# Performance work log

Hardware: AMD Instinct MI355X
Metric: run time of the kernel (lower is better)

## Reference

```python
import jax, jax.numpy as jnp
import numpy as np

NUM_HEADS = 16


def setup_inputs() -> dict:
    key = jax.random.key(0)
    ks = jax.random.split(key, 5)
    B, S, D = 4, 2048, 1024
    scale = 1.0 / np.sqrt(D)
    return {
        "x": jax.random.normal(ks[0], (B, S, D), dtype=jnp.float32),
        "q_proj": jax.random.normal(ks[1], (D, D), dtype=jnp.float32) * scale,
        "k_proj": jax.random.normal(ks[2], (D, D), dtype=jnp.float32) * scale,
        "v_proj": jax.random.normal(ks[3], (D, D), dtype=jnp.float32) * scale,
        "o_proj": jax.random.normal(ks[4], (D, D), dtype=jnp.float32) * scale,
    }


def reference(x, q_proj, k_proj, v_proj, o_proj):
    B, S, D = x.shape
    H = NUM_HEADS
    hd = D // H
    # projections: weight is [d_out, d_in]
    q = jnp.einsum('bsd,kd->bsk', x, q_proj)
    k = jnp.einsum('bsd,kd->bsk', x, k_proj)
    v = jnp.einsum('bsd,kd->bsk', x, v_proj)
    # split heads: [B, H, S, hd]
    q = q.reshape(B, S, H, hd).transpose(0, 2, 1, 3)
    k = k.reshape(B, S, H, hd).transpose(0, 2, 1, 3)
    v = v.reshape(B, S, H, hd).transpose(0, 2, 1, 3)
    scores = jnp.einsum('bhqd,bhkd->bhqk', q, k) / jnp.sqrt(jnp.asarray(hd, dtype=x.dtype))
    causal = jnp.tril(jnp.ones((S, S), dtype=bool))  # True = keep
    scores = jnp.where(causal, scores, -jnp.inf)
    attn = jax.nn.softmax(scores, axis=-1)
    out = jnp.einsum('bhqk,bhkd->bhqd', attn, v)
    out = out.transpose(0, 2, 1, 3).reshape(B, S, D)
    return jnp.einsum('bsv,mv->bsm', out, o_proj)
```

## Files before the change

### kernel.cpp

```cpp
#include <hip/hip_runtime.h>
#include <hip/hip_bf16.h>
#include <stdint.h>


typedef __bf16 bf16x8 __attribute__((ext_vector_type(8)));
typedef __bf16 bf16x4 __attribute__((ext_vector_type(4)));
typedef float  f32x4  __attribute__((ext_vector_type(4)));

static __device__ __forceinline__ f32x4 mfma16(bf16x8 a, bf16x8 b, f32x4 c) {
  return __builtin_amdgcn_mfma_f32_16x16x32_bf16(a, b, c, 0, 0, 0);
}

static __device__ __forceinline__ void load16_lds(const void* g, void* l) {
  __builtin_amdgcn_global_load_lds(
      (const __attribute__((address_space(1))) unsigned int*)g,
      (__attribute__((address_space(3))) unsigned int*)l, 16, 0, 0);
}

__global__ __launch_bounds__(256) void cvt_f32_bf16(
    const float* __restrict__ in, __bf16* __restrict__ out, int n8) {
  int i = blockIdx.x * blockDim.x + threadIdx.x;
  if (i >= n8) return;
  const float4* in4 = (const float4*)in;
  float4 a = in4[2 * i], b = in4[2 * i + 1];
  __bf16 v[8];
  v[0] = (__bf16)a.x; v[1] = (__bf16)a.y; v[2] = (__bf16)a.z; v[3] = (__bf16)a.w;
  v[4] = (__bf16)b.x; v[5] = (__bf16)b.y; v[6] = (__bf16)b.z; v[7] = (__bf16)b.w;
  *(bf16x8*)(out + 8 * i) = *(bf16x8*)v;
}

__global__ __launch_bounds__(256) void cvt_w(
    const float* __restrict__ w0, const float* __restrict__ w1,
    const float* __restrict__ w2, const float* __restrict__ w3,
    __bf16* __restrict__ wqkv, __bf16* __restrict__ wo) {
  int blk = blockIdx.x;
  int m = blk >> 9;
  const float* src = (m == 0) ? w0 : (m == 1) ? w1 : (m == 2) ? w2 : w3;
  __bf16* dst = (m < 3) ? (wqkv + (size_t)m * (1024 * 1024)) : wo;
  int i = (blk & 511) * 256 + threadIdx.x;
  const float4* in4 = (const float4*)src;
  float4 a = in4[2 * i], b = in4[2 * i + 1];
  __bf16 v[8];
  v[0] = (__bf16)a.x; v[1] = (__bf16)a.y; v[2] = (__bf16)a.z; v[3] = (__bf16)a.w;
  v[4] = (__bf16)b.x; v[5] = (__bf16)b.y; v[6] = (__bf16)b.z; v[7] = (__bf16)b.w;
  *(bf16x8*)(dst + 8 * i) = *(bf16x8*)v;
}

template <typename OutT>
__global__ __launch_bounds__(256) void gemm_bt2(
    const __bf16* __restrict__ A, const __bf16* __restrict__ Bw,
    OutT* __restrict__ C, int M, int N, int K) {
  __shared__ __align__(16) __bf16 As[128 * 32];
  __shared__ __align__(16) __bf16 Bs[128 * 32];
  const int t = threadIdx.x;
  const int lane = t & 63, w = t >> 6;
  const int wm = w >> 1, wn = w & 1;
  const int l15 = lane & 15, quad = lane >> 4;
  const long rowA0 = (long)blockIdx.y * 128;
  const long rowB0 = (long)blockIdx.x * 128;

  const int r0 = w * 32 + (lane >> 2);
  const int r1 = r0 + 16;
  const int c0 = (lane & 3) ^ ((r0 >> 1) & 3);
  const int c1 = (lane & 3) ^ ((r1 >> 1) & 3);
  const __bf16* pA0 = A + (rowA0 + r0) * (long)K + c0 * 8;
  const __bf16* pA1 = A + (rowA0 + r1) * (long)K + c1 * 8;
  const __bf16* pB0 = Bw + (rowB0 + r0) * (long)K + c0 * 8;
  const __bf16* pB1 = Bw + (rowB0 + r1) * (long)K + c1 * 8;
  __bf16* lA0 = As + (w * 32) * 32;
  __bf16* lA1 = As + (w * 32 + 16) * 32;
  __bf16* lB0 = Bs + (w * 32) * 32;
  __bf16* lB1 = Bs + (w * 32 + 16) * 32;

  int aoff[4], boff[4];
#pragma unroll
  for (int i = 0; i < 4; i++) {
    int Ra = wm * 64 + i * 16 + l15;
    aoff[i] = Ra * 32 + ((quad ^ ((Ra >> 1) & 3)) << 3);
    int Rb = wn * 64 + i * 16 + l15;
    boff[i] = Rb * 32 + ((quad ^ ((Rb >> 1) & 3)) << 3);
  }

  f32x4 acc[4][4] = {};
  for (int k0 = 0; k0 < K; k0 += 32) {
    load16_lds(pA0, lA0); load16_lds(pA1, lA1);
    load16_lds(pB0, lB0); load16_lds(pB1, lB1);
    pA0 += 32; pA1 += 32; pB0 += 32; pB1 += 32;
    __syncthreads();
    bf16x8 af[4], bfr[4];
#pragma unroll
    for (int i = 0; i < 4; i++) af[i] = *(const bf16x8*)(As + aoff[i]);
#pragma unroll
    for (int i = 0; i < 4; i++) bfr[i] = *(const bf16x8*)(Bs + boff[i]);
#pragma unroll
    for (int mt = 0; mt < 4; mt++)
#pragma unroll
      for (int nt = 0; nt < 4; nt++)
        acc[mt][nt] = mfma16(af[mt], bfr[nt], acc[mt][nt]);
    __syncthreads();
  }

#pragma unroll
  for (int mt = 0; mt < 4; mt++)
#pragma unroll
    for (int nt = 0; nt < 4; nt++)
#pragma unroll
      for (int r = 0; r < 4; r++) {
        long row = rowA0 + wm * 64 + mt * 16 + quad * 4 + r;
        long col = rowB0 + wn * 64 + nt * 16 + l15;
        float v = acc[mt][nt][r];
        if constexpr (sizeof(OutT) == 2) C[row * N + col] = (OutT)(__bf16)v;
        else                             C[row * N + col] = v;
      }
}

__global__ __launch_bounds__(256) void vtrans(
    const __bf16* __restrict__ QKV, __bf16* __restrict__ VT) {
  constexpr int LDs = 136;
  __shared__ __align__(16) __bf16 Ts[64 * LDs];
  const int t = threadIdx.x;
  const int st0 = blockIdx.x * 128, h = blockIdx.y, b = blockIdx.z;
  const long vbase = (long)b * 2048 * 3072 + 2048 + h * 64;
#pragma unroll
  for (int i = 0; i < 4; i++) {
    int sl = i * 32 + (t >> 3), d0 = (t & 7) * 8;
    __bf16 tmp[8];
    *(uint4*)tmp = *(const uint4*)(QKV + vbase + (long)(st0 + sl) * 3072 + d0);
#pragma unroll
    for (int j = 0; j < 8; j++) Ts[(d0 + j) * LDs + sl] = tmp[j];
  }
  __syncthreads();
  const long obase = (long)(b * 16 + h) * 64 * 2048 + st0;
  const int d = t >> 2;
#pragma unroll
  for (int i = 0; i < 4; i++) {
    int sc = ((t & 3) + 4 * i) * 8;
    *(uint4*)(VT + obase + (long)d * 2048 + sc) = *(const uint4*)(Ts + d * LDs + sc);
  }
}

__global__ __launch_bounds__(256) void attn4(
    const __bf16* __restrict__ QKV, const __bf16* __restrict__ VT,
    __bf16* __restrict__ O) {
  constexpr int SD = 3072;
  constexpr int LDP = 72;
  __shared__ __align__(16) __bf16 Ks[64 * 64];
  __shared__ __align__(16) __bf16 Vs[64 * 64];
  __shared__ __align__(16) __bf16 Pw[4 * 32 * LDP];
  const int t = threadIdx.x;
  const int lane = t & 63, w = t >> 6;
  const int l15 = lane & 15, quad = lane >> 4;
  const int jj = blockIdx.x, h = blockIdx.y, b = blockIdx.z;
  const long qbase = (long)b * 2048 * SD + h * 64;
  const long kbase = qbase + 1024;
  const long vtbase = (long)(b * 16 + h) * 64 * 2048;
  __bf16* Pme = Pw + w * 32 * LDP;

  const int sr = w * 16 + (lane >> 3);
  const int scg = (lane & 7) ^ (sr & 7);
  __bf16* ldsK0 = Ks + (w * 16) * 64;
  __bf16* ldsK1 = Ks + (w * 16 + 8) * 64;
  __bf16* ldsV0 = Vs + (w * 16) * 64;
  __bf16* ldsV1 = Vs + (w * 16 + 8) * 64;

  int kvoff[4][2];
#pragma unroll
  for (int nt = 0; nt < 4; nt++)
#pragma unroll
    for (int kk = 0; kk < 2; kk++)
      kvoff[nt][kk] = (nt * 16 + l15) * 64 + (((kk * 4 + quad) ^ (l15 & 7)) << 3);

#pragma unroll
  for (int half = 0; half < 2; half++) {
    const int qt = half ? (15 - jj) : jj;
    const int q0 = qt * 128;
    const int wrow0 = q0 + w * 32;

    bf16x8 qf[2][2];
#pragma unroll
    for (int mt = 0; mt < 2; mt++)
#pragma unroll
      for (int kk = 0; kk < 2; kk++)
        qf[mt][kk] = *(const bf16x8*)(QKV + qbase +
            (long)(wrow0 + mt * 16 + l15) * SD + kk * 32 + quad * 8);

    f32x4 o_acc[2][4] = {};
    float l_part[2] = {0.f, 0.f};

    const int nkt = 2 * qt + 2;
    for (int kt = 0; kt < nkt; kt++) {
      const int k0 = kt * 64;
      load16_lds(QKV + kbase + (long)(k0 + sr) * SD + scg * 8, ldsK0);
      load16_lds(QKV + kbase + (long)(k0 + sr + 8) * SD + scg * 8, ldsK1);
      load16_lds(VT + vtbase + (long)sr * 2048 + k0 + scg * 8, ldsV0);
      load16_lds(VT + vtbase + (long)(sr + 8) * 2048 + k0 + scg * 8, ldsV1);
      __syncthreads();

      if (k0 <= wrow0 + 31) {
        bf16x8 kf[4][2];
#pragma unroll
        for (int nt = 0; nt < 4; nt++)
#pragma unroll
          for (int kk = 0; kk < 2; kk++)
            kf[nt][kk] = *(const bf16x8*)(Ks + kvoff[nt][kk]);
        f32x4 st[4][2];
#pragma unroll
        for (int nt = 0; nt < 4; nt++)
#pragma unroll
          for (int mt = 0; mt < 2; mt++) {
            f32x4 z = {0.f, 0.f, 0.f, 0.f};
            z = mfma16(kf[nt][0], qf[mt][0], z);
            st[nt][mt] = mfma16(kf[nt][1], qf[mt][1], z);
          }
        const bool needmask = (k0 + 63 > wrow0);
#pragma unroll
        for (int mt = 0; mt < 2; mt++) {
          const int qrow = wrow0 + mt * 16 + l15;
#pragma unroll
          for (int nt = 0; nt < 4; nt++) {
            const int keyb = k0 + nt * 16 + quad * 4;
            bf16x4 pb;
#pragma unroll
            for (int r = 0; r < 4; r++) {
              float e = __expf(st[nt][mt][r] * 0.125f);
              if (needmask && (keyb + r > qrow)) e = 0.f;
              l_part[mt] += e;
              pb[r] = (__bf16)e;
            }
            *(bf16x4*)(Pme + (mt * 16 + l15) * LDP + nt * 16 + quad * 4) = pb;
          }
        }
#pragma unroll
        for (int kk = 0; kk < 2; kk++) {
          bf16x8 vf[4];
#pragma unroll
          for (int dt = 0; dt < 4; dt++)
            vf[dt] = *(const bf16x8*)(Vs + kvoff[dt][kk]);
#pragma unroll
          for (int mt = 0; mt < 2; mt++) {
            bf16x8 pf = *(const bf16x8*)(Pme + (mt * 16 + l15) * LDP + kk * 32 + quad * 8);
#pragma unroll
            for (int dt = 0; dt < 4; dt++)
              o_acc[mt][dt] = mfma16(pf, vf[dt], o_acc[mt][dt]);
          }
        }
      }
      __syncthreads();
    }

#pragma unroll
    for (int mt = 0; mt < 2; mt++) {
      float l = l_part[mt];
      l += __shfl_xor(l, 16, 64);
      l += __shfl_xor(l, 32, 64);
#pragma unroll
      for (int r = 0; r < 4; r++) {
        float lr = __shfl(l, quad * 4 + r, 64);
        float inv = 1.f / lr;
        int row = wrow0 + mt * 16 + quad * 4 + r;
        long ob = ((long)b * 2048 + row) * 1024 + h * 64;
#pragma unroll
        for (int dt = 0; dt < 4; dt++)
          O[ob + dt * 16 + l15] = (__bf16)(o_acc[mt][dt][r] * inv);
      }
    }
  }
}

extern "C" void kernel_launch(void* const* d_in, const int* in_sizes, int n_in,
                              void* d_out, int out_size, void* d_ws, size_t ws_size,
                              hipStream_t stream) {
  const float* x  = (const float*)d_in[0];
  const float* wq = (const float*)d_in[1];
  const float* wk = (const float*)d_in[2];
  const float* wv = (const float*)d_in[3];
  const float* wo = (const float*)d_in[4];
  float* out = (float*)d_out;

  char* ws = (char*)d_ws;
  __bf16* xb   = (__bf16*)(ws);
  __bf16* wqkv = (__bf16*)(ws + (16l << 20));
  __bf16* wob  = (__bf16*)(ws + (22l << 20));
  __bf16* QKV  = (__bf16*)(ws + (24l << 20));
  __bf16* VT   = (__bf16*)(ws + (72l << 20));
  __bf16* Ab   = xb;

  cvt_f32_bf16<<<4096, 256, 0, stream>>>(x, xb, 8192 * 1024 / 8);
  cvt_w<<<2048, 256, 0, stream>>>(wq, wk, wv, wo, wqkv, wob);

  gemm_bt2<__bf16><<<dim3(24, 64), 256, 0, stream>>>(xb, wqkv, QKV, 8192, 3072, 1024);

  vtrans<<<dim3(16, 16, 4), 256, 0, stream>>>(QKV, VT);

  attn4<<<dim3(8, 16, 4), 256, 0, stream>>>(QKV, VT, Ab);

  gemm_bt2<float><<<dim3(8, 64), 256, 0, stream>>>(Ab, wob, out, 8192, 1024, 1024);
}
```

Before: 277.4 us.

## Double-buffer K/V tiles in attention and fold softmax scale into Q weights

Converts the attention kernel's K/V LDS staging to a double buffer, so the next tile's global-to-LDS load is issued before computing on the current one. This overlaps memory latency with MFMA work and drops one barrier per iteration. The 1/sqrt(hd)*log2(e) factor is folded into the Q weight conversion, so the inner loop uses raw exp2 with no multiply, and a mask-free path handles fully unmasked tiles. The row-sum is computed by an extra MFMA against a ones vector instead of per-element adds and shuffles, and s_setprio hints are added around MFMA blocks. The cost is twice the K/V LDS, which may lower occupancy, and extra MFMA work for the row-sum.

```diff
diff --git a/kernel.cpp b/kernel.cpp
--- a/kernel.cpp
+++ b/kernel.cpp
@@ -37,12 +37,15 @@
   int m = blk >> 9;
   const float* src = (m == 0) ? w0 : (m == 1) ? w1 : (m == 2) ? w2 : w3;
   __bf16* dst = (m < 3) ? (wqkv + (size_t)m * (1024 * 1024)) : wo;
+  const float scl = (m == 0) ? 0.18033688011112042f : 1.0f;
   int i = (blk & 511) * 256 + threadIdx.x;
   const float4* in4 = (const float4*)src;
   float4 a = in4[2 * i], b = in4[2 * i + 1];
   __bf16 v[8];
-  v[0] = (__bf16)a.x; v[1] = (__bf16)a.y; v[2] = (__bf16)a.z; v[3] = (__bf16)a.w;
-  v[4] = (__bf16)b.x; v[5] = (__bf16)b.y; v[6] = (__bf16)b.z; v[7] = (__bf16)b.w;
+  v[0] = (__bf16)(a.x * scl); v[1] = (__bf16)(a.y * scl);
+  v[2] = (__bf16)(a.z * scl); v[3] = (__bf16)(a.w * scl);
+  v[4] = (__bf16)(b.x * scl); v[5] = (__bf16)(b.y * scl);
+  v[6] = (__bf16)(b.z * scl); v[7] = (__bf16)(b.w * scl);
   *(bf16x8*)(dst + 8 * i) = *(bf16x8*)v;
 }
 
@@ -144,8 +147,8 @@
     __bf16* __restrict__ O) {
   constexpr int SD = 3072;
   constexpr int LDP = 72;
-  __shared__ __align__(16) __bf16 Ks[64 * 64];
-  __shared__ __align__(16) __bf16 Vs[64 * 64];
+  __shared__ __align__(16) __bf16 Ks[2][64 * 64];
+  __shared__ __align__(16) __bf16 Vs[2][64 * 64];
   __shared__ __align__(16) __bf16 Pw[4 * 32 * LDP];
   const int t = threadIdx.x;
   const int lane = t & 63, w = t >> 6;
@@ -158,10 +161,9 @@
 
   const int sr = w * 16 + (lane >> 3);
   const int scg = (lane & 7) ^ (sr & 7);
-  __bf16* ldsK0 = Ks + (w * 16) * 64;
-  __bf16* ldsK1 = Ks + (w * 16 + 8) * 64;
-  __bf16* ldsV0 = Vs + (w * 16) * 64;
-  __bf16* ldsV1 = Vs + (w * 16 + 8) * 64;
+  const int ldsOff = (w * 16) * 64;
+  const __bf16* gK = QKV + kbase + (long)sr * SD + scg * 8;
+  const __bf16* gV = VT + vtbase + (long)sr * 2048 + scg * 8;
 
   int kvoff[4][2];
 #pragma unroll
@@ -169,6 +171,10 @@
 #pragma unroll
     for (int kk = 0; kk < 2; kk++)
       kvoff[nt][kk] = (nt * 16 + l15) * 64 + (((kk * 4 + quad) ^ (l15 & 7)) << 3);
+
+  bf16x8 ones;
+#pragma unroll
+  for (int j = 0; j < 8; j++) ones[j] = (__bf16)1.0f;
 
 #pragma unroll
   for (int half = 0; half < 2; half++) {
@@ -185,25 +191,42 @@
             (long)(wrow0 + mt * 16 + l15) * SD + kk * 32 + quad * 8);
 
     f32x4 o_acc[2][4] = {};
-    float l_part[2] = {0.f, 0.f};
+    f32x4 o_l[2] = {};
 
     const int nkt = 2 * qt + 2;
+
+    __syncthreads();
+    load16_lds(gK, Ks[0] + ldsOff);
+    load16_lds(gK + 8 * SD, Ks[0] + ldsOff + 8 * 64);
+    load16_lds(gV, Vs[0] + ldsOff);
+    load16_lds(gV + 8 * 2048, Vs[0] + ldsOff + 8 * 64);
+
+    int cur = 0;
     for (int kt = 0; kt < nkt; kt++) {
+      __syncthreads();
+      if (kt + 1 < nkt) {
+        const __bf16* gKn = gK + (long)(kt + 1) * 64 * SD;
+        const __bf16* gVn = gV + (kt + 1) * 64;
+        __bf16* lk = Ks[cur ^ 1] + ldsOff;
+        __bf16* lv = Vs[cur ^ 1] + ldsOff;
+        load16_lds(gKn, lk);
+        load16_lds(gKn + 8 * SD, lk + 8 * 64);
+        load16_lds(gVn, lv);
+        load16_lds(gVn + 8 * 2048, lv + 8 * 64);
+      }
+
       const int k0 = kt * 64;
-      load16_lds(QKV + kbase + (long)(k0 + sr) * SD + scg * 8, ldsK0);
-      load16_lds(QKV + kbase + (long)(k0 + sr + 8) * SD + scg * 8, ldsK1);
-      load16_lds(VT + vtbase + (long)sr * 2048 + k0 + scg * 8, ldsV0);
-      load16_lds(VT + vtbase + (long)(sr + 8) * 2048 + k0 + scg * 8, ldsV1);
-      __syncthreads();
-
       if (k0 <= wrow0 + 31) {
+        const __bf16* KsB = Ks[cur];
+        const __bf16* VsB = Vs[cur];
         bf16x8 kf[4][2];
 #pragma unroll
         for (int nt = 0; nt < 4; nt++)
 #pragma unroll
           for (int kk = 0; kk < 2; kk++)
-            kf[nt][kk] = *(const bf16x8*)(Ks + kvoff[nt][kk]);
+            kf[nt][kk] = *(const bf16x8*)(KsB + kvoff[nt][kk]);
         f32x4 st[4][2];
+        __builtin_amdgcn_s_setprio(1);
 #pragma unroll
         for (int nt = 0; nt < 4; nt++)
 #pragma unroll
@@ -212,51 +235,64 @@
             z = mfma16(kf[nt][0], qf[mt][0], z);
             st[nt][mt] = mfma16(kf[nt][1], qf[mt][1], z);
           }
-        const bool needmask = (k0 + 63 > wrow0);
-#pragma unroll
-        for (int mt = 0; mt < 2; mt++) {
-          const int qrow = wrow0 + mt * 16 + l15;
-#pragma unroll
-          for (int nt = 0; nt < 4; nt++) {
-            const int keyb = k0 + nt * 16 + quad * 4;
-            bf16x4 pb;
-#pragma unroll
-            for (int r = 0; r < 4; r++) {
-              float e = __expf(st[nt][mt][r] * 0.125f);
-              if (needmask && (keyb + r > qrow)) e = 0.f;
-              l_part[mt] += e;
-              pb[r] = (__bf16)e;
+        __builtin_amdgcn_s_setprio(0);
+
+        if (k0 + 63 <= wrow0) {
+#pragma unroll
+          for (int mt = 0; mt < 2; mt++)
+#pragma unroll
+            for (int nt = 0; nt < 4; nt++) {
+              bf16x4 pb;
+#pragma unroll
+              for (int r = 0; r < 4; r++)
+                pb[r] = (__bf16)__builtin_amdgcn_exp2f(st[nt][mt][r]);
+              *(bf16x4*)(Pme + (mt * 16 + l15) * LDP + nt * 16 + quad * 4) = pb;
             }
-            *(bf16x4*)(Pme + (mt * 16 + l15) * LDP + nt * 16 + quad * 4) = pb;
+        } else {
+#pragma unroll
+          for (int mt = 0; mt < 2; mt++) {
+            const int qrow = wrow0 + mt * 16 + l15;
+#pragma unroll
+            for (int nt = 0; nt < 4; nt++) {
+              const int keyb = k0 + nt * 16 + quad * 4;
+              bf16x4 pb;
+#pragma unroll
+              for (int r = 0; r < 4; r++) {
+                float e = __builtin_amdgcn_exp2f(st[nt][mt][r]);
+                if (keyb + r > qrow) e = 0.f;
+                pb[r] = (__bf16)e;
+              }
+              *(bf16x4*)(Pme + (mt * 16 + l15) * LDP + nt * 16 + quad * 4) = pb;
+            }
           }
         }
+
 #pragma unroll
         for (int kk = 0; kk < 2; kk++) {
           bf16x8 vf[4];
 #pragma unroll
           for (int dt = 0; dt < 4; dt++)
-            vf[dt] = *(const bf16x8*)(Vs + kvoff[dt][kk]);
+            vf[dt] = *(const bf16x8*)(VsB + kvoff[dt][kk]);
 #pragma unroll
           for (int mt = 0; mt < 2; mt++) {
             bf16x8 pf = *(const bf16x8*)(Pme + (mt * 16 + l15) * LDP + kk * 32 + quad * 8);
+            __builtin_amdgcn_s_setprio(1);
 #pragma unroll
             for (int dt = 0; dt < 4; dt++)
               o_acc[mt][dt] = mfma16(pf, vf[dt], o_acc[mt][dt]);
+            o_l[mt] = mfma16(pf, ones, o_l[mt]);
+            __builtin_amdgcn_s_setprio(0);
           }
         }
       }
-      __syncthreads();
+      cur ^= 1;
     }
 
 #pragma unroll
     for (int mt = 0; mt < 2; mt++) {
-      float l = l_part[mt];
-      l += __shfl_xor(l, 16, 64);
-      l += __shfl_xor(l, 32, 64);
 #pragma unroll
       for (int r = 0; r < 4; r++) {
-        float lr = __shfl(l, quad * 4 + r, 64);
-        float inv = 1.f / lr;
+        float inv = 1.f / o_l[mt][r];
         int row = wrow0 + mt * 16 + quad * 4 + r;
         long ob = ((long)b * 2048 + row) * 1024 + h * 64;
 #pragma unroll
```

After: 266.1 us. 4.1% less time.
